# Performance work log

Hardware: AMD Instinct MI355X
Metric: run time of the kernel (lower is better)

The kernel has to match this reference:

```python
import jax, jax.numpy as jnp
import numpy as np

N_FFT = 2048
HOP = 512
K = N_FFT // 2 + 1  # 1025 output frequency bins


def _dft_window_weights(n_fft):
    """Windowed real/imag DFT matrices, matching librosa hann (periodic) window
    and W[j,k] = exp(-2*pi*i*j*k/n_fft); conv weight = (W[:, :K] * win[:, None]).T."""
    n = np.arange(n_fft)
    win = 0.5 - 0.5 * np.cos(2.0 * np.pi * n / n_fft)  # hann, fftbins=True
    k = np.arange(n_fft // 2 + 1)
    ang = 2.0 * np.pi * np.outer(k, n) / n_fft  # (K, n_fft)
    w_real = np.cos(ang) * win[None, :]
    w_imag = -np.sin(ang) * win[None, :]
    return (jnp.asarray(w_real, jnp.float32), jnp.asarray(w_imag, jnp.float32))


def setup_inputs() -> dict:
    key = jax.random.key(0)
    x = jax.random.normal(key, (16, 2, 262144), dtype=jnp.float32)
    w_real, w_imag = _dft_window_weights(N_FFT)
    return {"x": x, "w_real": w_real, "w_imag": w_imag}


def reference(x, w_real, w_imag):
    B, C, L = x.shape
    pad = N_FFT // 2
    xp = jnp.pad(x, ((0, 0), (0, 0), (pad, pad)), mode="reflect")  # center=True
    T = (L + 2 * pad - N_FFT) // HOP + 1  # number of frames
    idx = HOP * jnp.arange(T)[:, None] + jnp.arange(N_FFT)[None, :]  # (T, n_fft)
    frames = xp[:, :, idx]  # (B, C, T, n_fft)
    # Windowed DFT as GEMM (same math as the conv-as-DFT in the torch module).
    real = jnp.einsum("bctn,kn->bckt", frames, w_real)  # (B, C, K, T)
    imag = jnp.einsum("bctn,kn->bckt", frames, w_imag)
    # torch.cat over channel dim -> (B, C*K, T), channel-major order
    real = real.reshape(B, C * K, T)
    imag = imag.reshape(B, C * K, T)
    return (real, imag)
```

## Files before the change

kernel.cpp:

```cpp
#include <hip/hip_runtime.h>

#define NFFT  2048
#define KF    1025
#define MROWS 2050
#define TT    513
#define HOPS  512
#define LSIG  262144
#define PADL  1024
#define XPADN 264192
#define XDN   66048
#define IMOFF (16 * MROWS * TT)
#define NBC   32
#define APL   262144

typedef __attribute__((ext_vector_type(8))) short bf16x8;
typedef __attribute__((ext_vector_type(4))) short bf16x4;
typedef __attribute__((ext_vector_type(4))) float f32x4;

__device__ __forceinline__ short f2bf(float f) {
    union { float f; unsigned u; } v; v.f = f;
    unsigned r = v.u + 0x7fffu + ((v.u >> 16) & 1u);
    return (short)(r >> 16);
}

typedef __attribute__((address_space(1))) void gas_void;
typedef __attribute__((address_space(3))) void las_void;

__device__ __forceinline__ void gload_lds16(const short* g, short* l) {
    __builtin_amdgcn_global_load_lds((gas_void*)(void*)const_cast<short*>(g),
                                     (las_void*)(void*)l, 16, 0, 0);
}

__global__ __launch_bounds__(256)
void prep_x(const float* __restrict__ x, short* __restrict__ xpad,
            short* __restrict__ xd) {
    const int bc = blockIdx.y;
    const int j4 = (blockIdx.x * 256 + threadIdx.x) * 4;
    const float* xb = x + (size_t)bc * LSIG;
    float4 v;
    if (j4 >= PADL && j4 + 4 <= PADL + LSIG) {
        v = *(const float4*)(xb + (j4 - PADL));
    } else {
        float t[4];
#pragma unroll
        for (int e = 0; e < 4; e++) {
            int s = j4 + e - PADL;
            if (s < 0) s = -s;
            if (s >= LSIG) s = 2 * LSIG - 2 - s;
            t[e] = xb[s];
        }
        v = make_float4(t[0], t[1], t[2], t[3]);
    }
    bf16x4 b = { f2bf(v.x), f2bf(v.y), f2bf(v.z), f2bf(v.w) };
    *(bf16x4*)(xpad + (size_t)bc * XPADN + j4) = b;
    const int j = j4 >> 2;
#pragma unroll
    for (int r = 0; r < 4; r++)
        xd[((size_t)r * NBC + bc) * XDN + j] = b[r];
}

__global__ __launch_bounds__(256)
void prep_basis2(const float* __restrict__ wr, const float* __restrict__ wi,
                 short* __restrict__ A) {
    const int r   = blockIdx.y;
    const int row = blockIdx.x;
    const float* w = ((row & 1) ? wi : wr) + (size_t)(row >> 1) * NFFT + r;
    short* dst = A + ((size_t)r * 512 + row) * 512;
    for (int m = threadIdx.x; m < 512; m += 256)
        dst[m] = f2bf(w[4 * m]);
}

__global__ __launch_bounds__(256, 1)
void stft_gemm_f(const short* __restrict__ Ab, const short* __restrict__ xd,
                 float* __restrict__ out) {
    extern __shared__ short lds[];

    const int tid  = threadIdx.x;
    const int lane = tid & 63;
    const int r    = tid >> 6;
    const int bcg  = blockIdx.x;
    const int mBase = blockIdx.y * 64;
    const int t0    = blockIdx.z * 64;

    const int l16  = lane & 15;
    const int quad = lane >> 4;
    const int lrow = lane >> 3;
    const int csrc = (lane & 7) ^ lrow;
    const int r7   = l16 & 7;

    short* strip = lds + r * 16384;

    const short* aSrc = Ab + (size_t)r * APL + (size_t)(mBase + lrow) * 512 + csrc * 8;
    const short* bPlane = xd + ((size_t)r * NBC + bcg) * XDN + csrc * 8;
    const short* bSrc[8];
#pragma unroll
    for (int i = 0; i < 8; i++) {
        int bt = t0 + 8 * i + lrow; if (bt > 512) bt = 512;
        bSrc[i] = bPlane + (size_t)bt * 128;
    }

    f32x4 acc[4][4];
#pragma unroll
    for (int i = 0; i < 4; i++)
#pragma unroll
        for (int j = 0; j < 4; j++)
            acc[i][j] = (f32x4){0.f, 0.f, 0.f, 0.f};

#pragma unroll
    for (int i = 0; i < 8; i++) {
        gload_lds16(aSrc + i * 4096, strip + i * 512);
        gload_lds16(bSrc[i],         strip + 8192 + i * 512);
    }

    for (int kt = 0; kt < 512; kt += 64) {
        const int cur = (kt >> 6) & 1;
        if (kt < 448) {
            short* dA = strip + ((cur ^ 1) << 12);
            short* dB = strip + 8192 + ((cur ^ 1) << 12);
            const int ko = kt + 64;
#pragma unroll
            for (int i = 0; i < 8; i++) {
                gload_lds16(aSrc + i * 4096 + ko, dA + i * 512);
                gload_lds16(bSrc[i] + ko,         dB + i * 512);
            }
            asm volatile("s_waitcnt vmcnt(16)" ::: "memory");
        } else {
            asm volatile("s_waitcnt vmcnt(0)" ::: "memory");
        }
        __builtin_amdgcn_sched_barrier(0);
        const short* Ac = strip + (cur << 12);
        const short* Bc = strip + 8192 + (cur << 12);
#pragma unroll
        for (int kk = 0; kk < 2; kk++) {
            const int p = (kk * 4 + quad) ^ r7;
            bf16x8 af[4], bfr[4];
#pragma unroll
            for (int i = 0; i < 4; i++)
                af[i] = *(const bf16x8*)(Ac + (i * 16 + l16) * 64 + p * 8);
#pragma unroll
            for (int j = 0; j < 4; j++)
                bfr[j] = *(const bf16x8*)(Bc + (j * 16 + l16) * 64 + p * 8);
#pragma unroll
            for (int i = 0; i < 4; i++)
#pragma unroll
                for (int j = 0; j < 4; j++)
                    acc[i][j] = __builtin_amdgcn_mfma_f32_16x16x32_bf16(
                        af[i], bfr[j], acc[i][j], 0, 0, 0);
        }
    }

    __syncthreads();
    float* sf = (float*)lds;
    float* Sr = sf + r * (64 * 66);
#pragma unroll
    for (int i = 0; i < 4; i++)
#pragma unroll
        for (int j = 0; j < 4; j++)
#pragma unroll
            for (int rr = 0; rr < 4; rr++)
                Sr[(i * 16 + quad * 4 + rr) * 66 + j * 16 + l16] = acc[i][j][rr];
    __syncthreads();

    float* oRe = out + (size_t)bcg * KF * TT;
    float* oIm = out + (size_t)IMOFF + (size_t)bcg * KF * TT;
    const int tg = t0 + lane;
    if (tg < TT) {
#pragma unroll
        for (int kl = 0; kl < 8; kl++) {
            const int kap = r * 8 + kl;
            const int kg  = (mBase >> 1) + kap;
            float u0 = sf[0 * 4224 + (2 * kap) * 66 + lane];
            float v0 = sf[0 * 4224 + (2 * kap + 1) * 66 + lane];
            float u1 = sf[1 * 4224 + (2 * kap) * 66 + lane];
            float v1 = sf[1 * 4224 + (2 * kap + 1) * 66 + lane];
            float u2 = sf[2 * 4224 + (2 * kap) * 66 + lane];
            float v2 = sf[2 * 4224 + (2 * kap + 1) * 66 + lane];
            float u3 = sf[3 * 4224 + (2 * kap) * 66 + lane];
            float v3 = sf[3 * 4224 + (2 * kap + 1) * 66 + lane];
            const float Eu = u0 + u2, Epu = u0 - u2;
            const float Ou = u1 + u3, Opu = u1 - u3;
            const float Ev = v0 + v2, Epv = v0 - v2;
            const float Ov = v1 + v3, Opv = v1 - v3;
            const size_t rA = (size_t)kg * TT + tg;
            const size_t rB = (size_t)(kg + 512) * TT + tg;
            const size_t rC = (size_t)(512 - kg) * TT + tg;
            const size_t rD = (size_t)(1024 - kg) * TT + tg;
            oRe[rA] = Eu + Ou;    oIm[rA] = Ev + Ov;
            oRe[rB] = Epu + Opv;  oIm[rB] = Epv - Opu;
            oRe[rC] = Epu - Opv;  oIm[rC] = -(Epv + Opu);
            oRe[rD] = Eu - Ou;    oIm[rD] = -(Ev - Ov);
        }
    }
}

__global__ __launch_bounds__(256)
void stft_tail(const float* __restrict__ wr, const float* __restrict__ wi,
               const short* __restrict__ xpad, float* __restrict__ out) {
    const int tb  = blockIdx.x;
    const int bc  = blockIdx.y;
    const int tid = threadIdx.x;
    const int lane = tid & 63;
    const int wid  = tid >> 6;
    const int l16  = lane & 15;
    const int quad = lane >> 4;

    const int t0 = (tb * 4 + wid) * 16;
    const int ls = l16 & 3;
    const int k  = 256 + (ls & 1) * 512;
    const float* bp = ((ls & 2) ? wi : wr) + (size_t)k * NFFT + quad * 8;
    const int tr = min(t0 + l16, 512);
    const short* ap = xpad + (size_t)bc * XPADN + (size_t)tr * HOPS + quad * 8;
    f32x4 acc0 = {0.f, 0.f, 0.f, 0.f}, acc1 = {0.f, 0.f, 0.f, 0.f};
    for (int kt = 0; kt < NFFT; kt += 64) {
        bf16x8 a0 = *(const bf16x8*)(ap + kt);
        bf16x8 a1 = *(const bf16x8*)(ap + kt + 32);
        float4 f0 = *(const float4*)(bp + kt), f1 = *(const float4*)(bp + kt + 4);
        float4 g0 = *(const float4*)(bp + kt + 32), g1 = *(const float4*)(bp + kt + 36);
        bf16x8 b0 = { f2bf(f0.x), f2bf(f0.y), f2bf(f0.z), f2bf(f0.w),
                      f2bf(f1.x), f2bf(f1.y), f2bf(f1.z), f2bf(f1.w) };
        bf16x8 b1 = { f2bf(g0.x), f2bf(g0.y), f2bf(g0.z), f2bf(g0.w),
                      f2bf(g1.x), f2bf(g1.y), f2bf(g1.z), f2bf(g1.w) };
        acc0 = __builtin_amdgcn_mfma_f32_16x16x32_bf16(a0, b0, acc0, 0, 0, 0);
        acc1 = __builtin_amdgcn_mfma_f32_16x16x32_bf16(a1, b1, acc1, 0, 0, 0);
    }
    if (l16 < 4) {
        size_t base = ((ls & 2) ? (size_t)IMOFF : 0) + (size_t)(bc * KF + k) * TT;
#pragma unroll
        for (int rr = 0; rr < 4; rr++) {
            int t = t0 + quad * 4 + rr;
            if (t < TT) out[base + t] = acc0[rr] + acc1[rr];
        }
    }
}

extern "C" void kernel_launch(void* const* d_in, const int* in_sizes, int n_in,
                              void* d_out, int out_size, void* d_ws, size_t ws_size,
                              hipStream_t stream) {
    const float* x  = (const float*)d_in[0];
    const float* wr = (const float*)d_in[1];
    const float* wi = (const float*)d_in[2];
    float* out = (float*)d_out;

    char* ws = (char*)d_ws;
    short* xpad = (short*)ws;
    short* xd   = (short*)(ws + 16908288);
    short* Ab   = (short*)(ws + 33816576);

    static bool cfgDone = false;
    if (!cfgDone) {
        (void)hipFuncSetAttribute((const void*)stft_gemm_f,
                                  hipFuncAttributeMaxDynamicSharedMemorySize,
                                  131072);
        cfgDone = true;
    }

    prep_x<<<dim3(258, NBC), 256, 0, stream>>>(x, xpad, xd);
    prep_basis2<<<dim3(512, 4), 256, 0, stream>>>(wr, wi, Ab);
    stft_gemm_f<<<dim3(NBC, 8, 9), 256, 131072, stream>>>(Ab, xd, out);
    stft_tail<<<dim3(9, NBC), 256, 0, stream>>>(wr, wi, xpad, out);
}
```

Baseline: 293.4 us.

## Halve GEMM K-tile to fit two blocks per CU and swizzle block order

The GEMM kernel's K-step drops from 64 to 32, which shrinks the per-wave LDS strip so each block needs about 68 KB instead of 128 KB. Launch bounds now allow two blocks per CU. The 3D grid is flattened to 1D with a remap that groups 8 M-tiles of the same signal/time tile together, aiming for better L2 reuse of the input frames. The cost is twice as many loop iterations and barriers, each with fewer MFMAs to hide load latency behind.

Result: slower. 299.8 us (+2.2%).

```diff
diff --git a/kernel.cpp b/kernel.cpp
--- a/kernel.cpp
+++ b/kernel.cpp
@@ -70,33 +70,37 @@
         dst[m] = f2bf(w[4 * m]);
 }
 
-__global__ __launch_bounds__(256, 1)
+__global__ __launch_bounds__(256, 2)
 void stft_gemm_f(const short* __restrict__ Ab, const short* __restrict__ xd,
                  float* __restrict__ out) {
     extern __shared__ short lds[];
 
+    const int bid = blockIdx.x;
+    const int g   = (bid & 7) + 8 * (bid >> 6);
+    const int y   = (bid >> 3) & 7;
+    const int bcg = g & 31;
+    const int z   = g >> 5;
+    const int mBase = y * 64;
+    const int t0    = z * 64;
+
     const int tid  = threadIdx.x;
     const int lane = tid & 63;
     const int r    = tid >> 6;
-    const int bcg  = blockIdx.x;
-    const int mBase = blockIdx.y * 64;
-    const int t0    = blockIdx.z * 64;
 
     const int l16  = lane & 15;
     const int quad = lane >> 4;
-    const int lrow = lane >> 3;
-    const int csrc = (lane & 7) ^ lrow;
-    const int r7   = l16 & 7;
-
-    short* strip = lds + r * 16384;
-
-    const short* aSrc = Ab + (size_t)r * APL + (size_t)(mBase + lrow) * 512 + csrc * 8;
+    const int lrow = lane >> 2;
+    const int csrc = (lane & 3) ^ (lrow & 3);
+
+    short* strip = lds + r * 8192;
+
+    const short* aRow = Ab + (size_t)r * APL + (size_t)(mBase + lrow) * 512 + csrc * 8;
     const short* bPlane = xd + ((size_t)r * NBC + bcg) * XDN + csrc * 8;
-    const short* bSrc[8];
-#pragma unroll
-    for (int i = 0; i < 8; i++) {
-        int bt = t0 + 8 * i + lrow; if (bt > 512) bt = 512;
-        bSrc[i] = bPlane + (size_t)bt * 128;
+    const short* bRow[4];
+#pragma unroll
+    for (int i = 0; i < 4; i++) {
+        int bt = t0 + 16 * i + lrow; if (bt > 512) bt = 512;
+        bRow[i] = bPlane + (size_t)bt * 128;
     }
 
     f32x4 acc[4][4];
@@ -106,47 +110,45 @@
         for (int j = 0; j < 4; j++)
             acc[i][j] = (f32x4){0.f, 0.f, 0.f, 0.f};
 
-#pragma unroll
-    for (int i = 0; i < 8; i++) {
-        gload_lds16(aSrc + i * 4096, strip + i * 512);
-        gload_lds16(bSrc[i],         strip + 8192 + i * 512);
-    }
-
-    for (int kt = 0; kt < 512; kt += 64) {
-        const int cur = (kt >> 6) & 1;
-        if (kt < 448) {
-            short* dA = strip + ((cur ^ 1) << 12);
-            short* dB = strip + 8192 + ((cur ^ 1) << 12);
-            const int ko = kt + 64;
-#pragma unroll
-            for (int i = 0; i < 8; i++) {
-                gload_lds16(aSrc + i * 4096 + ko, dA + i * 512);
-                gload_lds16(bSrc[i] + ko,         dB + i * 512);
+    const int lsw = (l16 & 3);
+
+#pragma unroll
+    for (int i = 0; i < 4; i++) {
+        gload_lds16(aRow + i * 8192, strip + i * 512);
+        gload_lds16(bRow[i],         strip + 2048 + i * 512);
+    }
+
+    for (int kt = 0; kt < 512; kt += 32) {
+        const int cur = (kt >> 5) & 1;
+        if (kt < 480) {
+            short* d = strip + ((cur ^ 1) << 12);
+            const int ko = kt + 32;
+#pragma unroll
+            for (int i = 0; i < 4; i++) {
+                gload_lds16(aRow + i * 8192 + ko, d + i * 512);
+                gload_lds16(bRow[i] + ko,         d + 2048 + i * 512);
             }
-            asm volatile("s_waitcnt vmcnt(16)" ::: "memory");
+            asm volatile("s_waitcnt vmcnt(8)" ::: "memory");
         } else {
             asm volatile("s_waitcnt vmcnt(0)" ::: "memory");
         }
         __builtin_amdgcn_sched_barrier(0);
         const short* Ac = strip + (cur << 12);
-        const short* Bc = strip + 8192 + (cur << 12);
-#pragma unroll
-        for (int kk = 0; kk < 2; kk++) {
-            const int p = (kk * 4 + quad) ^ r7;
-            bf16x8 af[4], bfr[4];
-#pragma unroll
-            for (int i = 0; i < 4; i++)
-                af[i] = *(const bf16x8*)(Ac + (i * 16 + l16) * 64 + p * 8);
+        const short* Bc = Ac + 2048;
+        bf16x8 af[4], bfr[4];
+#pragma unroll
+        for (int i = 0; i < 4; i++)
+            af[i] = *(const bf16x8*)(Ac + (i * 16 + l16) * 32 + ((quad ^ lsw) * 8));
+#pragma unroll
+        for (int j = 0; j < 4; j++)
+            bfr[j] = *(const bf16x8*)(Bc + (j * 16 + l16) * 32 + ((quad ^ lsw) * 8));
+#pragma unroll
+        for (int i = 0; i < 4; i++)
 #pragma unroll
             for (int j = 0; j < 4; j++)
-                bfr[j] = *(const bf16x8*)(Bc + (j * 16 + l16) * 64 + p * 8);
-#pragma unroll
-            for (int i = 0; i < 4; i++)
-#pragma unroll
-                for (int j = 0; j < 4; j++)
-                    acc[i][j] = __builtin_amdgcn_mfma_f32_16x16x32_bf16(
-                        af[i], bfr[j], acc[i][j], 0, 0, 0);
-        }
+                acc[i][j] = __builtin_amdgcn_mfma_f32_16x16x32_bf16(
+                    af[i], bfr[j], acc[i][j], 0, 0, 0);
+        __builtin_amdgcn_sched_barrier(0);
     }
 
     __syncthreads();
@@ -250,12 +252,12 @@
     if (!cfgDone) {
         (void)hipFuncSetAttribute((const void*)stft_gemm_f,
                                   hipFuncAttributeMaxDynamicSharedMemorySize,
-                                  131072);
+                                  69632);
         cfgDone = true;
     }
 
     prep_x<<<dim3(258, NBC), 256, 0, stream>>>(x, xpad, xd);
     prep_basis2<<<dim3(512, 4), 256, 0, stream>>>(wr, wi, Ab);
-    stft_gemm_f<<<dim3(NBC, 8, 9), 256, 131072, stream>>>(Ab, xd, out);
+    stft_gemm_f<<<dim3(2304), 256, 69632, stream>>>(Ab, xd, out);
     stft_tail<<<dim3(9, NBC), 256, 0, stream>>>(wr, wi, xpad, out);
 }
```
